# Kernel tuning notes

Measured on AMD Instinct MI355X. Metric: run time of the kernel, lower is better.

Reference implementation:

```python
import jax, jax.numpy as jnp
import numpy as np

T, B, E, H = 2048, 4, 1024, 16
EH = E // H  # 64


def setup_inputs() -> dict:
    rng = jax.random.key(0)
    ks = jax.random.split(rng, 8)
    s = 0.02  # weight init scale to keep softmax logits reasonable
    return {
        "query": jax.random.normal(ks[0], (T, B, E), jnp.float32),
        "key": jax.random.normal(ks[1], (T, B, E), jnp.float32),
        "value": jax.random.normal(ks[2], (T, B, E), jnp.float32),
        "mask": jax.random.uniform(ks[3], (T, T), jnp.float32),
        "w_qkv": jax.random.normal(ks[4], (3 * E, E), jnp.float32) * s,
        "b_qkv": jax.random.normal(ks[5], (3 * E,), jnp.float32) * s,
        "w_out": jax.random.normal(ks[6], (E, E), jnp.float32) * s,
        "b_out": jax.random.normal(ks[7], (E,), jnp.float32) * s,
    }


def reference(query, key, value, mask, w_qkv, b_qkv, w_out, b_out):
    # query/key/value: [T, B, E] (sequence-first, as in the torch module)
    t, b, e = query.shape
    eh = e // H
    wq, wk, wv = jnp.split(w_qkv, 3, axis=0)  # each [E, E]
    bq, bk, bv = jnp.split(b_qkv, 3, axis=0)

    def proj_heads(x, w, bias):
        y = x @ w.T + bias                    # [T, B, E]
        # [T,B,H,Eh] -> [B,H,T,Eh]  (matches unflatten/transpose/permute chain)
        return y.reshape(t, b, H, eh).transpose(1, 2, 0, 3)

    q = proj_heads(query, wq, bq)             # [B, H, T, Eh]
    k = proj_heads(key, wk, bk)
    v = proj_heads(value, wv, bv)

    scale = 1.0 / np.sqrt(eh).astype(np.float32)
    scores = jnp.einsum('bhqd,bhkd->bhqk', q, k) * scale   # [B,H,T,T]
    scores = scores * mask[None, None, :, :]               # multiplicative mask
    # is_causal=False, attn_mask=None -> attn_bias is zeros (skip identity add)
    attn = jax.nn.softmax(scores, axis=-1)
    # dropout=0.0 -> identity
    ctx = jnp.einsum('bhqk,bhkd->bhqd', attn, v)           # [B,H,T,Eh]
    ctx = ctx.transpose(0, 2, 1, 3).reshape(b, t, e)       # [B,T,E]
    out = ctx @ w_out.T + b_out                            # [B,T,E]
    return out.transpose(1, 0, 2)                          # [T,B,E]
```

## Files before the change

### kernel.cpp

```cpp
#include <hip/hip_runtime.h>
#include <hip/hip_bf16.h>
#include <stdint.h>

#define T_DIM 2048
#define B_DIM 4
#define E_DIM 1024
#define H_DIM 16
#define EHD 64
#define L2E 1.4426950408889634f
#define QSCALE (0.125f * L2E)
#define FMAXC 12.0f

typedef __attribute__((ext_vector_type(8))) short bf16x8;
typedef __attribute__((ext_vector_type(4))) float f32x4;
typedef __attribute__((ext_vector_type(2))) float f32x2;
typedef __attribute__((ext_vector_type(2))) unsigned u32x2;

__device__ __forceinline__ unsigned short f2bf(float x) {
  unsigned int u = __builtin_bit_cast(unsigned int, x);
  u += 0x7fffu + ((u >> 16) & 1u);
  return (unsigned short)(u >> 16);
}

__device__ __forceinline__ unsigned pkbf(float a, float b) {
  return (unsigned)f2bf(a) | ((unsigned)f2bf(b) << 16);
}

__device__ __forceinline__ unsigned pkbf2(float a, float b) {
  unsigned ua = __builtin_bit_cast(unsigned, a) + 0x8000u;
  unsigned ub = __builtin_bit_cast(unsigned, b) + 0x8000u;
  return (ua >> 16) | (ub & 0xffff0000u);
}

__device__ __forceinline__ f32x2 bfpair(unsigned w) {
  u32x2 u = {w << 16, w & 0xffff0000u};
  return __builtin_bit_cast(f32x2, u);
}

__device__ __forceinline__ void gload16(const void* g, void* l) {
  __builtin_amdgcn_global_load_lds(
      (const __attribute__((address_space(1))) void*)g,
      (__attribute__((address_space(3))) void*)l, 16, 0, 0);
}

__global__ __launch_bounds__(256) void cvt_kernel(const float4* __restrict__ in,
                                                  uint2* __restrict__ out, int n4) {
  int i = blockIdx.x * 256 + threadIdx.x;
  int stride = gridDim.x * 256;
  for (; i < n4; i += stride) {
    float4 f = in[i];
    uint2 o;
    o.x = pkbf(f.x, f.y);
    o.y = pkbf(f.z, f.w);
    out[i] = o;
  }
}

template <int MODE>
__global__ __launch_bounds__(256) void gemm_kernel(
    const unsigned short* __restrict__ Abase,
    const unsigned short* __restrict__ Bt,
    const float* __restrict__ bias,
    void* __restrict__ outv, int K) {
  __shared__ alignas(16) short As[128 * 32];
  __shared__ alignas(16) short Bs[128 * 32];
  const int tid = threadIdx.x;
  const int lane = tid & 63, wave = tid >> 6;
  const int m0 = blockIdx.x * 128, n0 = blockIdx.y * 128;
  const int wr = wave >> 1, wc = wave & 1;
  const int lrow = lane & 15, lgrp = lane >> 4;

  const unsigned short* A = Abase;
  if (MODE == 0) A += (size_t)(n0 >> 10) * (8192u * 1024u);

  f32x4 acc[4][4];
#pragma unroll
  for (int m = 0; m < 4; ++m)
#pragma unroll
    for (int n = 0; n < 4; ++n) acc[m][n] = (f32x4){0.f, 0.f, 0.f, 0.f};

  const int srow = wave * 16 + (lane >> 2);
  const int scol = (lane & 3) * 8;
  short* lA0 = As + wave * 16 * 32;
  short* lA1 = As + (64 + wave * 16) * 32;
  short* lB0 = Bs + wave * 16 * 32;
  short* lB1 = Bs + (64 + wave * 16) * 32;

  for (int k0 = 0; k0 < K; k0 += 32) {
    const unsigned short* ga = A + (size_t)(m0 + srow) * K + k0 + scol;
    const unsigned short* gb = Bt + (size_t)(n0 + srow) * K + k0 + scol;
    gload16(ga, lA0);
    gload16(ga + (size_t)64 * K, lA1);
    gload16(gb, lB0);
    gload16(gb + (size_t)64 * K, lB1);
    __syncthreads();
    const short* pa = As + (wr * 64 + lrow) * 32 + lgrp * 8;
    const short* pb = Bs + (wc * 64 + lrow) * 32 + lgrp * 8;
    bf16x8 a[4], b[4];
#pragma unroll
    for (int m = 0; m < 4; ++m) a[m] = *(const bf16x8*)(pa + m * 512);
#pragma unroll
    for (int n = 0; n < 4; ++n) b[n] = *(const bf16x8*)(pb + n * 512);
#pragma unroll
    for (int m = 0; m < 4; ++m)
#pragma unroll
      for (int n = 0; n < 4; ++n)
        acc[m][n] = __builtin_amdgcn_mfma_f32_16x16x32_bf16(a[m], b[n], acc[m][n], 0, 0, 0);
    __syncthreads();
  }

#pragma unroll
  for (int n = 0; n < 4; ++n) {
    const int gn = n0 + wc * 64 + n * 16 + lrow;
    const float bv = bias[gn];
    if (MODE == 0) {
      unsigned short* out = (unsigned short*)outv;
      const int which = gn >> 10;
      const float qsc = (which == 0) ? QSCALE : 1.0f;
      const int e = gn & 1023;
      const int hh = e >> 6, dd = e & 63;
#pragma unroll
      for (int m = 0; m < 4; ++m)
#pragma unroll
        for (int r = 0; r < 4; ++r) {
          const int gm = m0 + wr * 64 + m * 16 + lgrp * 4 + r;
          const int t = gm >> 2, bb = gm & 3;
          const unsigned short val = f2bf((acc[m][n][r] + bv) * qsc);
          if (which == 2) {
            out[((size_t)(2 * B_DIM * H_DIM) + bb * H_DIM + hh) * (T_DIM * EHD) +
                (size_t)(t >> 6) * 4096 + dd * 64 + (t & 63)] = val;
          } else {
            out[((size_t)which * B_DIM * H_DIM + bb * H_DIM + hh) * (T_DIM * EHD) +
                (size_t)t * EHD + dd] = val;
          }
        }
    } else {
      float* out = (float*)outv;
#pragma unroll
      for (int m = 0; m < 4; ++m)
#pragma unroll
        for (int r = 0; r < 4; ++r) {
          const int gm = m0 + wr * 64 + m * 16 + lgrp * 4 + r;
          const int bb = gm >> 11, t = gm & 2047;
          out[((size_t)t * B_DIM + bb) * E_DIM + gn] = acc[m][n][r] + bv;
        }
    }
  }
}

__global__ __launch_bounds__(256, 2) void attn_kernel(
    const unsigned short* __restrict__ Qm, const unsigned short* __restrict__ Km,
    const unsigned short* __restrict__ Vtm, const unsigned short* __restrict__ Mb,
    unsigned short* __restrict__ ctx) {
  __shared__ alignas(16) short Ks[2][4096];
  __shared__ alignas(16) short Vs[2][4096];
  __shared__ alignas(16) short Ml[2][8192];
  __shared__ alignas(16) short Pl[4][2][1024];
  const int tid = threadIdx.x, lane = tid & 63, wave = tid >> 6;
  const int lrow = lane & 15, lgrp = lane >> 4;
  const int bh = blockIdx.y, b = bh >> 4, h = bh & 15;
  const int q0 = blockIdx.x * 128;

  const size_t base = (size_t)bh * (T_DIM * EHD);

  bf16x8 qf0[2], qf1[2];
  int qrow[2];
#pragma unroll
  for (int g = 0; g < 2; ++g) {
    qrow[g] = q0 + g * 64 + wave * 16 + lrow;
    const unsigned short* qp = Qm + base + (size_t)qrow[g] * EHD + lgrp * 8;
    qf0[g] = *(const bf16x8*)qp;
    qf1[g] = *(const bf16x8*)(qp + 32);
  }

  f32x4 oacc[2][4];
#pragma unroll
  for (int g = 0; g < 2; ++g)
#pragma unroll
    for (int n = 0; n < 4; ++n) oacc[g][n] = (f32x4){0.f, 0.f, 0.f, 0.f};
  f32x2 racc[2] = {(f32x2){0.f, 0.f}, (f32x2){0.f, 0.f}};

  const int rr = lane >> 3;
  const int cs = (((lane & 7) ^ rr) * 8);
  const int r0w = wave * 8;
  const int rx = (lrow & 7) * 8;
  const int c0 = (lgrp * 8) ^ rx;

#define STAGE(bufi, kv0)                                                        \
  {                                                                             \
    _Pragma("unroll") for (int i = 0; i < 2; ++i) {                             \
      const int r0 = i * 32 + r0w;                                              \
      gload16(Km + base + (size_t)((kv0) + r0 + rr) * EHD + cs,                 \
              &Ks[bufi][r0 * 64]);                                              \
      gload16(Vtm + base + (size_t)(kv0) * EHD + (r0 + rr) * 64 + cs,           \
              &Vs[bufi][r0 * 64]);                                              \
    }                                                                           \
    _Pragma("unroll") for (int i = 0; i < 4; ++i) {                             \
      const int mrow = wave * 32 + i * 8;                                       \
      gload16(Mb + (size_t)(q0 + mrow + rr) * T_DIM + (kv0) + cs,               \
              &Ml[bufi][mrow * 64]);                                            \
    }                                                                           \
  }

  short* plw0 = &Pl[wave][0][lrow * 64];
  short* plw1 = &Pl[wave][1][lrow * 64];
  const int mrb0 = (wave * 16 + lrow) * 64;
  const int mrb1 = (64 + wave * 16 + lrow) * 64;
  const int msub = (lgrp & 1) * 4;
  const int mg0 = (lgrp >> 1);

#define ATTN_ITER(CUR, DO_PRE, TN)                                              \
  {                                                                             \
    if (DO_PRE) {                                                               \
      STAGE((CUR) ^ 1, (TN) * 64);                                              \
      __builtin_amdgcn_sched_barrier(0);                                        \
    }                                                                           \
    const short* kb = Ks[CUR];                                                  \
    const short* vb = Vs[CUR];                                                  \
    const short* mlb = Ml[CUR];                                                 \
    float sv[2][4][4];                                                          \
    __builtin_amdgcn_s_setprio(1);                                              \
    _Pragma("unroll") for (int n = 0; n < 4; ++n) {                             \
      const short* kp = kb + (n * 16 + lrow) * 64;                              \
      const bf16x8 kf0 = *(const bf16x8*)(kp + c0);                             \
      const bf16x8 kf1 = *(const bf16x8*)(kp + (c0 ^ 32));                      \
      f32x4 s0 = (f32x4){0.f, 0.f, 0.f, 0.f}, s1 = s0;                          \
      s0 = __builtin_amdgcn_mfma_f32_16x16x32_bf16(kf0, qf0[0], s0, 0, 0, 0);   \
      s0 = __builtin_amdgcn_mfma_f32_16x16x32_bf16(kf1, qf1[0], s0, 0, 0, 0);   \
      s1 = __builtin_amdgcn_mfma_f32_16x16x32_bf16(kf0, qf0[1], s1, 0, 0, 0);   \
      s1 = __builtin_amdgcn_mfma_f32_16x16x32_bf16(kf1, qf1[1], s1, 0, 0, 0);   \
      _Pragma("unroll") for (int r = 0; r < 4; ++r) {                           \
        sv[0][n][r] = s0[r];                                                    \
        sv[1][n][r] = s1[r];                                                    \
      }                                                                         \
    }                                                                           \
    __builtin_amdgcn_s_setprio(0);                                              \
    _Pragma("unroll") for (int g = 0; g < 2; ++g) {                             \
      short* plw = g ? plw1 : plw0;                                             \
      const int mrb = g ? mrb1 : mrb0;                                          \
      _Pragma("unroll") for (int n = 0; n < 4; ++n) {                           \
        const int mgr = (n * 2 + mg0) ^ (lrow & 7);                             \
        const uint2 mw = *(const uint2*)(mlb + mrb + mgr * 8 + msub);           \
        const f32x2 s01 = {sv[g][n][0], sv[g][n][1]};                           \
        const f32x2 s23 = {sv[g][n][2], sv[g][n][3]};                           \
        const f32x2 t01 = __builtin_elementwise_fma(                            \
            s01, bfpair(mw.x), (f32x2){-FMAXC, -FMAXC});                        \
        const f32x2 t23 = __builtin_elementwise_fma(                            \
            s23, bfpair(mw.y), (f32x2){-FMAXC, -FMAXC});                        \
        const float p0 = __builtin_amdgcn_exp2f(t01.x);                         \
        const float p1 = __builtin_amdgcn_exp2f(t01.y);                         \
        const float p2 = __builtin_amdgcn_exp2f(t23.x);                         \
        const float p3 = __builtin_amdgcn_exp2f(t23.y);                         \
        racc[g] += (f32x2){p0, p1} + (f32x2){p2, p3};                           \
        uint2 w;                                                                \
        w.x = pkbf2(p0, p1);                                                    \
        w.y = pkbf2(p2, p3);                                                    \
        *(uint2*)(plw + ((n * 16 + lgrp * 4) ^ rx)) = w;                        \
      }                                                                         \
    }                                                                           \
    __builtin_amdgcn_s_setprio(1);                                              \
    _Pragma("unroll") for (int kc = 0; kc < 2; ++kc) {                          \
      const int pc = ((kc * 32) + lgrp * 8) ^ rx;                               \
      const bf16x8 pB0 = *(const bf16x8*)(plw0 + pc);                           \
      const bf16x8 pB1 = *(const bf16x8*)(plw1 + pc);                           \
      _Pragma("unroll") for (int n = 0; n < 4; ++n) {                           \
        const bf16x8 vf = *(const bf16x8*)(vb + (n * 16 + lrow) * 64 + pc);     \
        oacc[0][n] = __builtin_amdgcn_mfma_f32_16x16x32_bf16(vf, pB0, oacc[0][n], 0, 0, 0); \
        oacc[1][n] = __builtin_amdgcn_mfma_f32_16x16x32_bf16(vf, pB1, oacc[1][n], 0, 0, 0); \
      }                                                                         \
    }                                                                           \
    __builtin_amdgcn_s_setprio(0);                                              \
  }

#define WAITBAR                                                                 \
  asm volatile("s_waitcnt vmcnt(0)" ::: "memory");                              \
  __builtin_amdgcn_sched_barrier(0);                                            \
  __builtin_amdgcn_s_barrier();                                                 \
  __builtin_amdgcn_sched_barrier(0);

  STAGE(0, 0);
  WAITBAR

  for (int tt = 0; tt < 15; ++tt) {
    ATTN_ITER(0, 1, 2 * tt + 1);
    WAITBAR
    ATTN_ITER(1, 1, 2 * tt + 2);
    WAITBAR
  }
  ATTN_ITER(0, 1, 31);
  WAITBAR
  ATTN_ITER(1, 0, 0);

#undef ATTN_ITER
#undef WAITBAR
#undef STAGE

#pragma unroll
  for (int g = 0; g < 2; ++g) {
    float lr = racc[g].x + racc[g].y;
    lr += __shfl_xor(lr, 16);
    lr += __shfl_xor(lr, 32);
    const float inv = 1.f / lr;
    unsigned short* cp =
        ctx + ((size_t)b * T_DIM + qrow[g]) * E_DIM + h * EHD + lgrp * 4;
#pragma unroll
    for (int n = 0; n < 4; ++n) {
      uint2 w;
      w.x = pkbf2(oacc[g][n][0] * inv, oacc[g][n][1] * inv);
      w.y = pkbf2(oacc[g][n][2] * inv, oacc[g][n][3] * inv);
      *(uint2*)(cp + n * 16) = w;
    }
  }
}

extern "C" void kernel_launch(void* const* d_in, const int* in_sizes, int n_in,
                              void* d_out, int out_size, void* d_ws, size_t ws_size,
                              hipStream_t stream) {
  const float* q    = (const float*)d_in[0];
  const float* k    = (const float*)d_in[1];
  const float* v    = (const float*)d_in[2];
  const float* mask = (const float*)d_in[3];
  const float* wqkv = (const float*)d_in[4];
  const float* bqkv = (const float*)d_in[5];
  const float* wout = (const float*)d_in[6];
  const float* bout = (const float*)d_in[7];

  char* ws = (char*)d_ws;
  unsigned short* Xb   = (unsigned short*)(ws);
  unsigned short* Wqb  = (unsigned short*)(ws + 50331648);
  unsigned short* Wob  = (unsigned short*)(ws + 56623104);
  unsigned short* QKVb = (unsigned short*)(ws + 58720256);
  unsigned short* CTXb = (unsigned short*)(ws);
  unsigned short* Mb   = (unsigned short*)(ws + 16777216);

  cvt_kernel<<<2048, 256, 0, stream>>>((const float4*)q, (uint2*)Xb, 2097152);
  cvt_kernel<<<2048, 256, 0, stream>>>((const float4*)k, (uint2*)(Xb + 8388608), 2097152);
  cvt_kernel<<<2048, 256, 0, stream>>>((const float4*)v, (uint2*)(Xb + 16777216), 2097152);
  cvt_kernel<<<1024, 256, 0, stream>>>((const float4*)wqkv, (uint2*)Wqb, 786432);
  cvt_kernel<<<512, 256, 0, stream>>>((const float4*)wout, (uint2*)Wob, 262144);

  gemm_kernel<0><<<dim3(64, 24), 256, 0, stream>>>(Xb, Wqb, bqkv, QKVb, 1024);
  cvt_kernel<<<1024, 256, 0, stream>>>((const float4*)mask, (uint2*)Mb, 1048576);
  attn_kernel<<<dim3(16, 64), 256, 0, stream>>>(QKVb, QKVb + 8388608,
                                                QKVb + 16777216, Mb, CTXb);
  gemm_kernel<1><<<dim3(64, 8), 256, 0, stream>>>(CTXb, Wob, bout, d_out, 1024);
}
```

Measured before the change: 283.8 us.

## Pre-permute mask into fragment order and fuse fp32-to-bf16 conversion launches

The five separate conversion launches become one fused kernel that picks its source tensor by index range, which removes launch gaps. A new mask_perm kernel writes the bf16 mask in the exact per-lane fragment order the attention kernel consumes. The attention kernel can then stage the mask with contiguous loads and read it with two 16-byte LDS loads per group instead of scattered swizzled 8-byte reads. P packing switches to truncation instead of round-to-nearest, which is slightly cheaper but loses a little precision, and the ctx output goes back to full round-to-nearest-even packing.

```diff
diff --git a/kernel.cpp b/kernel.cpp
--- a/kernel.cpp
+++ b/kernel.cpp
@@ -26,14 +26,13 @@
   return (unsigned)f2bf(a) | ((unsigned)f2bf(b) << 16);
 }
 
-__device__ __forceinline__ unsigned pkbf2(float a, float b) {
-  unsigned ua = __builtin_bit_cast(unsigned, a) + 0x8000u;
-  unsigned ub = __builtin_bit_cast(unsigned, b) + 0x8000u;
-  return (ua >> 16) | (ub & 0xffff0000u);
-}
-
-__device__ __forceinline__ f32x2 bfpair(unsigned w) {
-  u32x2 u = {w << 16, w & 0xffff0000u};
+__device__ __forceinline__ unsigned pk_trunc(float a, float b) {
+  return (__builtin_bit_cast(unsigned, a) >> 16) |
+         (__builtin_bit_cast(unsigned, b) & 0xffff0000u);
+}
+
+__device__ __forceinline__ f32x2 bfpair(unsigned lo, unsigned hi_w) {
+  u32x2 u = {lo << 16, hi_w & 0xffff0000u};
   return __builtin_bit_cast(f32x2, u);
 }
 
@@ -43,17 +42,51 @@
       (__attribute__((address_space(3))) void*)l, 16, 0, 0);
 }
 
-__global__ __launch_bounds__(256) void cvt_kernel(const float4* __restrict__ in,
-                                                  uint2* __restrict__ out, int n4) {
+__global__ __launch_bounds__(256) void cvt_fused(
+    const float4* __restrict__ q, const float4* __restrict__ k,
+    const float4* __restrict__ v, const float4* __restrict__ wqkv,
+    const float4* __restrict__ wout, uint2* __restrict__ xq,
+    uint2* __restrict__ xk, uint2* __restrict__ xv, uint2* __restrict__ wq,
+    uint2* __restrict__ wo) {
   int i = blockIdx.x * 256 + threadIdx.x;
-  int stride = gridDim.x * 256;
-  for (; i < n4; i += stride) {
-    float4 f = in[i];
+  const int stride = gridDim.x * 256;
+  for (; i < 7340032; i += stride) {
+    const float4* s;
+    uint2* d;
+    int j;
+    if (i < 2097152) { s = q; d = xq; j = i; }
+    else if (i < 4194304) { s = k; d = xk; j = i - 2097152; }
+    else if (i < 6291456) { s = v; d = xv; j = i - 4194304; }
+    else if (i < 7077888) { s = wqkv; d = wq; j = i - 6291456; }
+    else { s = wout; d = wo; j = i - 7077888; }
+    const float4 f = s[j];
     uint2 o;
     o.x = pkbf(f.x, f.y);
     o.y = pkbf(f.z, f.w);
-    out[i] = o;
-  }
+    d[j] = o;
+  }
+}
+
+__global__ __launch_bounds__(256) void mask_perm(const float* __restrict__ mask,
+                                                 uint4* __restrict__ out) {
+  const int c = blockIdx.x * 256 + threadIdx.x;
+  const int lane = c & 63;
+  const int g = (c >> 6) & 1;
+  const int wave = (c >> 7) & 3;
+  const int h = (c >> 9) & 1;
+  const int t = (c >> 10) & 31;
+  const int qblk = c >> 15;
+  const int lrow = lane & 15, lgrp = lane >> 4;
+  const int qq = qblk * 128 + g * 64 + wave * 16 + lrow;
+  const int k0 = t * 64 + h * 32 + lgrp * 4;
+  const float4 f0 = *(const float4*)(mask + (size_t)qq * T_DIM + k0);
+  const float4 f1 = *(const float4*)(mask + (size_t)qq * T_DIM + k0 + 16);
+  uint4 o;
+  o.x = pkbf(f0.x, f0.y);
+  o.y = pkbf(f0.z, f0.w);
+  o.z = pkbf(f1.x, f1.y);
+  o.w = pkbf(f1.z, f1.w);
+  out[c] = o;
 }
 
 template <int MODE>
@@ -162,6 +195,7 @@
   const int q0 = blockIdx.x * 128;
 
   const size_t base = (size_t)bh * (T_DIM * EHD);
+  const unsigned short* mbase = Mb + (size_t)blockIdx.x * 262144;
 
   bf16x8 qf0[2], qf1[2];
   int qrow[2];
@@ -186,33 +220,32 @@
   const int rx = (lrow & 7) * 8;
   const int c0 = (lgrp * 8) ^ rx;
 
-#define STAGE(bufi, kv0)                                                        \
+#define STAGE(bufi, T)                                                          \
   {                                                                             \
+    const int kv0 = (T) * 64;                                                   \
     _Pragma("unroll") for (int i = 0; i < 2; ++i) {                             \
       const int r0 = i * 32 + r0w;                                              \
-      gload16(Km + base + (size_t)((kv0) + r0 + rr) * EHD + cs,                 \
+      gload16(Km + base + (size_t)(kv0 + r0 + rr) * EHD + cs,                   \
               &Ks[bufi][r0 * 64]);                                              \
-      gload16(Vtm + base + (size_t)(kv0) * EHD + (r0 + rr) * 64 + cs,           \
+      gload16(Vtm + base + (size_t)kv0 * EHD + (r0 + rr) * 64 + cs,             \
               &Vs[bufi][r0 * 64]);                                              \
     }                                                                           \
-    _Pragma("unroll") for (int i = 0; i < 4; ++i) {                             \
-      const int mrow = wave * 32 + i * 8;                                       \
-      gload16(Mb + (size_t)(q0 + mrow + rr) * T_DIM + (kv0) + cs,               \
-              &Ml[bufi][mrow * 64]);                                            \
+    _Pragma("unroll") for (int h2 = 0; h2 < 2; ++h2) {                          \
+      _Pragma("unroll") for (int p = 0; p < 2; ++p) {                           \
+        const int sl = (h2 * 4 + wave) * 2 + p;                                 \
+        gload16(mbase + (size_t)(T) * 8192 + sl * 512 + lane * 8,               \
+                &Ml[bufi][sl * 512]);                                           \
+      }                                                                         \
     }                                                                           \
   }
 
   short* plw0 = &Pl[wave][0][lrow * 64];
   short* plw1 = &Pl[wave][1][lrow * 64];
-  const int mrb0 = (wave * 16 + lrow) * 64;
-  const int mrb1 = (64 + wave * 16 + lrow) * 64;
-  const int msub = (lgrp & 1) * 4;
-  const int mg0 = (lgrp >> 1);
 
 #define ATTN_ITER(CUR, DO_PRE, TN)                                              \
   {                                                                             \
     if (DO_PRE) {                                                               \
-      STAGE((CUR) ^ 1, (TN) * 64);                                              \
+      STAGE((CUR) ^ 1, TN);                                                     \
       __builtin_amdgcn_sched_barrier(0);                                        \
     }                                                                           \
     const short* kb = Ks[CUR];                                                  \
@@ -237,24 +270,29 @@
     __builtin_amdgcn_s_setprio(0);                                              \
     _Pragma("unroll") for (int g = 0; g < 2; ++g) {                             \
       short* plw = g ? plw1 : plw0;                                             \
-      const int mrb = g ? mrb1 : mrb0;                                          \
+      const uint4 m01 =                                                         \
+          *(const uint4*)(mlb + (wave * 2 + g) * 512 + lane * 8);               \
+      const uint4 m23 =                                                         \
+          *(const uint4*)(mlb + ((4 + wave) * 2 + g) * 512 + lane * 8);         \
+      const unsigned mwx[4] = {m01.x, m01.z, m23.x, m23.z};                     \
+      const unsigned mwy[4] = {m01.y, m01.w, m23.y, m23.w};                     \
       _Pragma("unroll") for (int n = 0; n < 4; ++n) {                           \
-        const int mgr = (n * 2 + mg0) ^ (lrow & 7);                             \
-        const uint2 mw = *(const uint2*)(mlb + mrb + mgr * 8 + msub);           \
         const f32x2 s01 = {sv[g][n][0], sv[g][n][1]};                           \
         const f32x2 s23 = {sv[g][n][2], sv[g][n][3]};                           \
+        const f32x2 m0v = bfpair(mwx[n], mwx[n]);                               \
+        const f32x2 m1v = bfpair(mwy[n], mwy[n]);                               \
         const f32x2 t01 = __builtin_elementwise_fma(                            \
-            s01, bfpair(mw.x), (f32x2){-FMAXC, -FMAXC});                        \
+            s01, m0v, (f32x2){-FMAXC, -FMAXC});                                 \
         const f32x2 t23 = __builtin_elementwise_fma(                            \
-            s23, bfpair(mw.y), (f32x2){-FMAXC, -FMAXC});                        \
+            s23, m1v, (f32x2){-FMAXC, -FMAXC});                                 \
         const float p0 = __builtin_amdgcn_exp2f(t01.x);                         \
         const float p1 = __builtin_amdgcn_exp2f(t01.y);                         \
         const float p2 = __builtin_amdgcn_exp2f(t23.x);                         \
         const float p3 = __builtin_amdgcn_exp2f(t23.y);                         \
         racc[g] += (f32x2){p0, p1} + (f32x2){p2, p3};                           \
         uint2 w;                                                                \
-        w.x = pkbf2(p0, p1);                                                    \
-        w.y = pkbf2(p2, p3);                                                    \
+        w.x = pk_trunc(p0, p1);                                                 \
+        w.y = pk_trunc(p2, p3);                                                 \
         *(uint2*)(plw + ((n * 16 + lgrp * 4) ^ rx)) = w;                        \
       }                                                                         \
     }                                                                           \
@@ -306,8 +344,8 @@
 #pragma unroll
     for (int n = 0; n < 4; ++n) {
       uint2 w;
-      w.x = pkbf2(oacc[g][n][0] * inv, oacc[g][n][1] * inv);
-      w.y = pkbf2(oacc[g][n][2] * inv, oacc[g][n][3] * inv);
+      w.x = pkbf(oacc[g][n][0] * inv, oacc[g][n][1] * inv);
+      w.y = pkbf(oacc[g][n][2] * inv, oacc[g][n][3] * inv);
       *(uint2*)(cp + n * 16) = w;
     }
   }
@@ -333,14 +371,14 @@
   unsigned short* CTXb = (unsigned short*)(ws);
   unsigned short* Mb   = (unsigned short*)(ws + 16777216);
 
-  cvt_kernel<<<2048, 256, 0, stream>>>((const float4*)q, (uint2*)Xb, 2097152);
-  cvt_kernel<<<2048, 256, 0, stream>>>((const float4*)k, (uint2*)(Xb + 8388608), 2097152);
-  cvt_kernel<<<2048, 256, 0, stream>>>((const float4*)v, (uint2*)(Xb + 16777216), 2097152);
-  cvt_kernel<<<1024, 256, 0, stream>>>((const float4*)wqkv, (uint2*)Wqb, 786432);
-  cvt_kernel<<<512, 256, 0, stream>>>((const float4*)wout, (uint2*)Wob, 262144);
+  cvt_fused<<<2048, 256, 0, stream>>>(
+      (const float4*)q, (const float4*)k, (const float4*)v,
+      (const float4*)wqkv, (const float4*)wout, (uint2*)Xb,
+      (uint2*)(Xb + 8388608), (uint2*)(Xb + 16777216), (uint2*)Wqb,
+      (uint2*)Wob);
 
   gemm_kernel<0><<<dim3(64, 24), 256, 0, stream>>>(Xb, Wqb, bqkv, QKVb, 1024);
-  cvt_kernel<<<1024, 256, 0, stream>>>((const float4*)mask, (uint2*)Mb, 1048576);
+  mask_perm<<<2048, 256, 0, stream>>>(mask, (uint4*)Mb);
   attn_kernel<<<dim3(16, 64), 256, 0, stream>>>(QKVb, QKVb + 8388608,
                                                 QKVb + 16777216, Mb, CTXb);
   gemm_kernel<1><<<dim3(64, 8), 256, 0, stream>>>(CTXb, Wob, bout, d_out, 1024);
```

After: 269.3 us. 5.1% less time.
